# Kernel tuning notes

Measured on AMD Instinct MI355X. Metric: run time of the kernel, lower is better.

## Reference

```python
import jax, jax.numpy as jnp
import numpy as np

B, Tc, E, K, M, V = 8, 1024, 256, 8, 2048, 16
T1 = Tc * K          # penultimate layer length = 8192
TLAST = M * K        # last layer length = 16384


def setup_inputs() -> dict:
    key = jax.random.key(0)
    ks = jax.random.split(key, 12)
    x = jax.random.normal(ks[0], (B, Tc, E), jnp.float32)
    # penultimate values: exactly M 'mixed' tokens (value==2) per row, rest in {1,3}
    base = jnp.where(jnp.arange(T1) < M, 2, 1 + 2 * jax.random.randint(ks[1], (B, T1), 0, 2))
    perm = jnp.argsort(jax.random.uniform(ks[2], (B, T1)), axis=1)
    val1 = jnp.take_along_axis(base, perm, axis=1)
    vallast = 1 + 2 * jax.random.randint(ks[3], (B, TLAST), 0, 2)
    value = jnp.concatenate([val1, vallast], axis=1).astype(jnp.int64)
    depth = jnp.concatenate([jnp.full((B, T1), 5), jnp.full((B, TLAST), 6)], axis=1).astype(jnp.int64)
    pos = jax.random.randint(ks[4], (B, T1 + TLAST, 3), 0, 64).astype(jnp.int64)
    s = 0.02
    W1 = s * jax.random.normal(ks[5], (E, E, K), jnp.float32)  # ConvTranspose1d weight [in,out,k]
    b1 = s * jax.random.normal(ks[6], (E,), jnp.float32)
    W0 = s * jax.random.normal(ks[7], (E, E, K), jnp.float32)
    b0 = s * jax.random.normal(ks[8], (E,), jnp.float32)
    Wl = s * jax.random.normal(ks[9], (V + 1, E), jnp.float32)
    bl = s * jax.random.normal(ks[10], (V + 1,), jnp.float32)
    return {"x": x, "value": value, "depth": depth, "pos": pos, "num_mix": M,
            "W1": W1, "b1": b1, "W0": W0, "b0": b0, "Wl": Wl, "bl": bl}


def _deconv(x, W, b):
    # ConvTranspose1d with kernel=stride=K: each token expands to K tokens
    n, t, e = x.shape
    o = W.shape[1]
    y = jnp.einsum('nte,eoj->ntjo', x, W)  # [N,T,K,O]
    return y.reshape(n, t * W.shape[2], o) + b


def reference(x, value, depth, pos, num_mix, W1, b1, W0, b0, Wl, bl):
    n, tc, e = x.shape
    k = W1.shape[2]
    t1 = tc * k
    max_depth = jnp.max(depth)
    len_1 = jnp.sum(depth == max_depth - 1, axis=1)               # [N]
    tt = jnp.arange(t1)
    val_1 = jnp.where(tt[None, :] < len_1[:, None], value[:, :t1], 0)  # padded penultimate values
    mix_mask = val_1 == 2                                         # [N,T1]
    mix_1 = jnp.sum(mix_mask, axis=1)                             # [N]
    y_1 = _deconv(x, W1, b1)                                      # [N,T1,E]
    # stable pack: bring positions with value==2 to the front, keep order
    order = jnp.argsort(jnp.where(mix_mask, 0, 1), axis=1, stable=True)
    sel = order[:, :num_mix]                                      # [N,M]
    x_0 = jnp.take_along_axis(y_1, sel[:, :, None], axis=1)       # [N,M,E]
    valid = (jnp.arange(num_mix)[None, :] < mix_1[:, None]).astype(x_0.dtype)
    x_0 = x_0 * valid[:, :, None]                                 # zero-pad beyond per-row mix count
    y_0 = _deconv(x_0, W0, b0)                                    # [N,M*K,E]
    return y_0 @ Wl.T + bl                                        # [N,M*K,V+1]
```

## Files before the change

kernel.cpp:

```cpp
#include <hip/hip_runtime.h>

typedef __attribute__((ext_vector_type(8))) short bf16x8;
typedef __attribute__((ext_vector_type(4))) float f32x4;

#define BB 8
#define TC 1024
#define EE 256
#define KJ 8
#define MSEL 2048
#define V1 17
#define T1 8192
#define TTOT 24576
#define BI_TOT 16384
#define NCOLP 160
#define WSTRIDE 264

#define SCAL_OFF 0
#define GRP_OFF  1024
#define WFT_OFF  (GRP_OFF + 524288)
#define B2_OFF   (WFT_OFF + NCOLP*WSTRIDE*2)
#define BF0_OFF  (B2_OFF + 640)
#define WCT_OFF  (BF0_OFF + 128)

__device__ __forceinline__ unsigned short f2bf(float f) {
    union { float f; unsigned u; } x; x.f = f;
    unsigned r = x.u + 0x7fffu + ((x.u >> 16) & 1u);
    return (unsigned short)(r >> 16);
}
__device__ __forceinline__ float bf2f(unsigned short h) {
    union { unsigned u; float f; } x; x.u = ((unsigned)h) << 16;
    return x.f;
}

__global__ __launch_bounds__(256) void k_pre(const float* W0, const float* Wl, const int* depth,
                                             unsigned short* wfT, int* scal) {
    int bid = blockIdx.x, tid = threadIdx.x;
    __shared__ float w0s[EE * KJ];
    __shared__ float wls[V1 * 257];
    __shared__ int s_red[4];
    int em = bid;
    for (int idx = tid; idx < EE * KJ; idx += 256) w0s[idx] = W0[em * EE * KJ + idx];
    for (int idx = tid; idx < V1 * EE; idx += 256) {
        int v = idx >> 8, o = idx & 255;
        wls[v * 257 + o] = Wl[idx];
    }
    __syncthreads();
    if (tid < 136) {
        int j = tid / V1, v = tid - j * V1;
        float acc = 0.f;
        #pragma unroll 4
        for (int o = 0; o < EE; ++o) acc += w0s[o * KJ + j] * wls[v * 257 + o];
        wfT[(j * 20 + v) * WSTRIDE + em] = f2bf(acc);
    }
    if (bid < 8) {
        int b = bid;
        if (b == 0 && tid < 8) scal[33 + tid] = 0;
        const int4* dp = (const int4*)(depth + b * TTOT);
        int m = -2147483648;
        for (int i = tid; i < 6144; i += 256) {
            int4 d = dp[i];
            m = max(max(m, max(d.x, d.y)), max(d.z, d.w));
        }
        #pragma unroll
        for (int dd = 32; dd; dd >>= 1) m = max(m, __shfl_down(m, dd, 64));
        if ((tid & 63) == 0) s_red[tid >> 6] = m;
        __syncthreads();
        int bmax = max(max(s_red[0], s_red[1]), max(s_red[2], s_red[3]));
        if (tid == 0) scal[1 + b] = bmax;
        int c1 = 0, c2 = 0;
        for (int i = tid; i < 6144; i += 256) {
            int4 d = dp[i];
            c1 += (d.x == bmax) + (d.y == bmax) + (d.z == bmax) + (d.w == bmax);
            c2 += (d.x == bmax - 1) + (d.y == bmax - 1) + (d.z == bmax - 1) + (d.w == bmax - 1);
        }
        int cc = (c1 << 16) + c2;
        #pragma unroll
        for (int dd = 32; dd; dd >>= 1) cc += __shfl_down(cc, dd, 64);
        __syncthreads();
        if ((tid & 63) == 0) s_red[tid >> 6] = cc;
        __syncthreads();
        if (tid == 0) {
            int tot = s_red[0] + s_red[1] + s_red[2] + s_red[3];
            scal[9 + b] = tot >> 16;
            scal[17 + b] = tot & 0xffff;
        }
    }
}

__global__ __launch_bounds__(256) void k_mid(
        const int* value, const float* W1, const float* b1, const float* b0,
        const float* Wl, const float* bl,
        int* scal, int* groups, const unsigned short* wfT, float* bias2, float* bf0,
        unsigned short* wct) {
    int bid = blockIdx.x, tid = threadIdx.x;
    __shared__ __align__(16) unsigned short b1s[32 * WSTRIDE];
    __shared__ __align__(16) unsigned short af[NCOLP * WSTRIDE];
    __shared__ int s_wt[4], s_lcnt[8], s_lcnt2[8], s_lbase[8];
    if (bid < 64) {
        int g = bid >> 3;
        int e0 = (bid & 7) * 32;
        {
            int em_l = tid & 63;
            int eb = (tid >> 6) * 8;
            #pragma unroll
            for (int i = 0; i < 8; ++i) {
                int e = eb + i;
                #pragma unroll
                for (int c = 0; c < 4; ++c) {
                    int em = c * 64 + em_l;
                    b1s[e * WSTRIDE + em] = f2bf(W1[(e0 + e) * (EE * KJ) + em * KJ + g]);
                }
            }
        }
        for (int idx = tid; idx < 5120; idx += 256) {
            int row = idx >> 5, f = idx & 31;
            ((int4*)af)[row * 33 + f] = ((const int4*)wfT)[row * 33 + f];
        }
        __syncthreads();

        int w = tid >> 6, l = tid & 63;
        int ntile = w & 1, mhalf = w >> 1;
        int lr = l & 15, lq = l >> 4;
        f32x4 acc[5];
        #pragma unroll
        for (int t = 0; t < 5; ++t) acc[t] = (f32x4){0.f, 0.f, 0.f, 0.f};

        #pragma unroll
        for (int ch = 0; ch < 4; ++ch) {
            #pragma unroll
            for (int s = 0; s < 2; ++s) {
                bf16x8 bfr = *(const bf16x8*)&b1s[(ntile * 16 + lr) * WSTRIDE + ch * 64 + s * 32 + lq * 8];
                #pragma unroll
                for (int t = 0; t < 5; ++t) {
                    bf16x8 afr = *(const bf16x8*)&af[((mhalf * 5 + t) * 16 + lr) * WSTRIDE + ch * 64 + s * 32 + lq * 8];
                    acc[t] = __builtin_amdgcn_mfma_f32_16x16x32_bf16(afr, bfr, acc[t], 0, 0, 0);
                }
            }
        }
        #pragma unroll
        for (int t = 0; t < 5; ++t) {
            int m = (mhalf * 5 + t) * 16 + lq * 4;
            int n = e0 + ntile * 16 + lr;
            #pragma unroll
            for (int r = 0; r < 4; ++r)
                wct[(g * NCOLP + m + r) * WSTRIDE + n] = f2bf(acc[t][r]);
        }
        if (bid == 0) {
            for (int c = tid; c < NCOLP; c += 256) {
                int vv = c % 20;
                float s = 0.f;
                if (vv < V1) {
                    for (int e8 = 0; e8 < 32; ++e8) {
                        bf16x8 a8 = *(const bf16x8*)&af[c * WSTRIDE + e8 * 8];
                        #pragma unroll
                        for (int u = 0; u < 8; ++u)
                            s += b1[e8 * 8 + u] * bf2f((unsigned short)a8[u]);
                    }
                }
                bias2[c] = s;
            }
        } else if (bid == 1) {
            if (tid < V1) {
                float s = 0.f;
                #pragma unroll 4
                for (int e = 0; e < EE; ++e) s += b0[e] * Wl[tid * EE + e];
                bf0[tid] = s + bl[tid];
            }
        }
    } else {
        int b = bid - 64;
        int mb = scal[1 + b], cm = scal[9 + b], cm1 = scal[17 + b];
        int gmax = scal[1];
        #pragma unroll
        for (int q = 2; q <= 8; ++q) gmax = max(gmax, scal[q]);
        int len1 = (mb == gmax) ? cm1 : ((mb == gmax - 1) ? cm : 0);
        const int* vb = value + b * TTOT;
        int t0 = tid * 32;
        unsigned mask = 0;
        #pragma unroll
        for (int k = 0; k < 32; k += 4) {
            int4 v = *(const int4*)(vb + t0 + k);
            if (t0 + k + 0 < len1 && v.x == 2) mask |= 1u << (k + 0);
            if (t0 + k + 1 < len1 && v.y == 2) mask |= 1u << (k + 1);
            if (t0 + k + 2 < len1 && v.z == 2) mask |= 1u << (k + 2);
            if (t0 + k + 3 < len1 && v.w == 2) mask |= 1u << (k + 3);
        }
        int cnt = __popc(mask);
        int inc = cnt;
        #pragma unroll
        for (int d = 1; d < 64; d <<= 1) {
            int n = __shfl_up(inc, d, 64);
            if ((tid & 63) >= d) inc += n;
        }
        int lane = tid & 63, wid = tid >> 6;
        if (lane == 63) s_wt[wid] = inc;
        if (tid < 8) { s_lcnt[tid] = 0; s_lcnt2[tid] = 0; }
        __syncthreads();
        int woff = 0;
        for (int w = 0; w < wid; ++w) woff += s_wt[w];
        int off0 = woff + inc - cnt;
        int mix1 = s_wt[0] + s_wt[1] + s_wt[2] + s_wt[3];
        int mix1c = min(mix1, MSEL);
        {
            int off = off0;
            #pragma unroll
            for (int k = 0; k < 32; ++k) {
                if (mask & (1u << k)) {
                    if (off < MSEL) atomicAdd(&s_lcnt[(t0 + k) & 7], 1);
                    off++;
                }
            }
        }
        if (tid == 0 && mix1c < MSEL) atomicAdd(&s_lcnt[0], MSEL - mix1c);
        __syncthreads();
        if (tid < 8) s_lbase[tid] = atomicAdd(&scal[33 + tid], s_lcnt[tid]);
        __syncthreads();
        {
            int off = off0;
            #pragma unroll
            for (int k = 0; k < 32; ++k) {
                if (mask & (1u << k)) {
                    if (off < MSEL) {
                        int t = t0 + k;
                        int g = t & 7;
                        int ls = atomicAdd(&s_lcnt2[g], 1);
                        groups[g * BI_TOT + s_lbase[g] + ls] =
                            ((b * MSEL + off) << 11) | ((t >> 3) << 1) | 1;
                    }
                    off++;
                }
            }
        }
        for (int i = mix1c + tid; i < MSEL; i += 256) {
            int ls = atomicAdd(&s_lcnt2[0], 1);
            groups[s_lbase[0] + ls] = (b * MSEL + i) << 11;
        }
    }
}

__global__ __launch_bounds__(256) void k_main(const float* x, const unsigned short* wct,
        const int* scal, const int* groups, const float* bias2, const float* bf0, float* out) {
    int g = blockIdx.x >> 5;
    int slot = blockIdx.x & 31;
    int cntg = scal[33 + g];
    if (slot * 32 >= cntg) return;

    __shared__ __align__(16) unsigned short xs[32 * WSTRIDE];
    __shared__ __align__(16) unsigned short wts[NCOLP * WSTRIDE];
    __shared__ int xoffs[2][32], obase[2][32];
    __shared__ unsigned char vflag[2][32];
    int tid = threadIdx.x;
    const int4* wsrc = (const int4*)wct;

    if (tid < 32) {
        int nrows = min(32, cntg - slot * 32);
        int flag = 0, xo = 0, ob = 0;
        if (tid < nrows) {
            int pk = groups[g * BI_TOT + slot * 32 + tid];
            int tq = (pk >> 1) & 1023;
            int bi = pk >> 11;
            xo = ((bi >> 11) * TC + tq) * EE;
            ob = bi * 136;
            flag = 1 + (pk & 1);
        }
        xoffs[0][tid] = xo; obase[0][tid] = ob; vflag[0][tid] = (unsigned char)flag;
    }
    for (int idx = tid; idx < 5120; idx += 256) {
        int row = idx >> 5, f = idx & 31;
        ((int4*)wts)[row * 33 + f] = wsrc[(g * NCOLP + row) * 33 + f];
    }
    __syncthreads();

    int w = tid >> 6, l = tid & 63;
    int rw = w & 1, chalf = w >> 1;
    int lr = l & 15, lq = l >> 4;
    int row8 = tid >> 3, q8 = tid & 7;

    float4 xr[8];
    {
        const float* xp = x + xoffs[0][row8];
        #pragma unroll
        for (int i = 0; i < 8; ++i) xr[i] = *(const float4*)(xp + (q8 + 8 * i) * 4);
    }

    int pp = 0;
    for (int tile = slot; tile * 32 < cntg; tile += 32, pp ^= 1) {
        #pragma unroll
        for (int i = 0; i < 8; ++i) {
            ushort4 pk;
            pk.x = f2bf(xr[i].x); pk.y = f2bf(xr[i].y);
            pk.z = f2bf(xr[i].z); pk.w = f2bf(xr[i].w);
            *(ushort4*)&xs[row8 * WSTRIDE + (q8 + 8 * i) * 4] = pk;
        }
        int ntile = tile + 32;
        int more = (ntile * 32 < cntg);
        if (more && tid < 32) {
            int nrows = min(32, cntg - ntile * 32);
            int flag = 0, xo = 0, ob = 0;
            if (tid < nrows) {
                int pk = groups[g * BI_TOT + ntile * 32 + tid];
                int tq = (pk >> 1) & 1023;
                int bi = pk >> 11;
                xo = ((bi >> 11) * TC + tq) * EE;
                ob = bi * 136;
                flag = 1 + (pk & 1);
            }
            xoffs[pp ^ 1][tid] = xo; obase[pp ^ 1][tid] = ob; vflag[pp ^ 1][tid] = (unsigned char)flag;
        }
        __syncthreads();
        if (more) {
            const float* xp = x + xoffs[pp ^ 1][row8];
            #pragma unroll
            for (int i = 0; i < 8; ++i) xr[i] = *(const float4*)(xp + (q8 + 8 * i) * 4);
        }

        f32x4 acc[5];
        #pragma unroll
        for (int t = 0; t < 5; ++t) acc[t] = (f32x4){0.f, 0.f, 0.f, 0.f};
        #pragma unroll
        for (int ch = 0; ch < 4; ++ch) {
            #pragma unroll
            for (int s = 0; s < 2; ++s) {
                bf16x8 afr = *(const bf16x8*)&xs[(rw * 16 + lr) * WSTRIDE + ch * 64 + s * 32 + lq * 8];
                #pragma unroll
                for (int t = 0; t < 5; ++t) {
                    bf16x8 bfr = *(const bf16x8*)&wts[((chalf * 5 + t) * 16 + lr) * WSTRIDE + ch * 64 + s * 32 + lq * 8];
                    acc[t] = __builtin_amdgcn_mfma_f32_16x16x32_bf16(afr, bfr, acc[t], 0, 0, 0);
                }
            }
        }
        #pragma unroll
        for (int t = 0; t < 5; ++t) {
            int col = (chalf * 5 + t) * 16 + lr;
            int j = col / 20, v = col % 20;
            if (v < V1) {
                float bb = bias2[col] + bf0[v];
                float b0v = bf0[v];
                #pragma unroll
                for (int r = 0; r < 4; ++r) {
                    int row = rw * 16 + lq * 4 + r;
                    int fl = vflag[pp][row];
                    if (fl) out[obase[pp][row] + j * V1 + v] = (fl == 2) ? (acc[t][r] + bb) : b0v;
                }
            }
        }
        __syncthreads();
    }
}

extern "C" void kernel_launch(void* const* d_in, const int* in_sizes, int n_in,
                              void* d_out, int out_size, void* d_ws, size_t ws_size,
                              hipStream_t stream) {
    const float* x     = (const float*)d_in[0];
    const int*   value = (const int*)d_in[1];
    const int*   depth = (const int*)d_in[2];
    const float* W1    = (const float*)d_in[5];
    const float* b1    = (const float*)d_in[6];
    const float* W0    = (const float*)d_in[7];
    const float* b0    = (const float*)d_in[8];
    const float* Wl    = (const float*)d_in[9];
    const float* bl    = (const float*)d_in[10];
    float* out = (float*)d_out;
    char* ws = (char*)d_ws;

    int*            scal   = (int*)(ws + SCAL_OFF);
    int*            groups = (int*)(ws + GRP_OFF);
    unsigned short* wfT    = (unsigned short*)(ws + WFT_OFF);
    float*          bias2  = (float*)(ws + B2_OFF);
    float*          bf0    = (float*)(ws + BF0_OFF);
    unsigned short* wct    = (unsigned short*)(ws + WCT_OFF);

    k_pre <<<dim3(256), dim3(256), 0, stream>>>(W0, Wl, depth, wfT, scal);
    k_mid <<<dim3(72),  dim3(256), 0, stream>>>(value, W1, b1, b0, Wl, bl,
                                                scal, groups, wfT, bias2, bf0, wct);
    k_main<<<dim3(256), dim3(256), 0, stream>>>(x, wct, scal, groups, bias2, bf0, out);
}
```

Measured before the change: 131.8 us.

## Stream weight slices through small LDS buffer and quadruple k_main grid

k_main now launches 1024 blocks, 128 tiles per group, instead of 256. It no longer keeps the full 160x256 bf16 weight matrix resident in LDS. Instead it streams the weights in four 64-wide K chunks through a small LDS buffer, prefetching into registers and adding extra barriers. The smaller LDS footprint and larger grid are meant to raise occupancy and parallelism, at the cost of reloading weights for every tile, more synchronisation, and dropping the cross-tile x prefetch.

```diff
diff --git a/kernel.cpp b/kernel.cpp
--- a/kernel.cpp
+++ b/kernel.cpp
@@ -240,93 +240,79 @@
 
 __global__ __launch_bounds__(256) void k_main(const float* x, const unsigned short* wct,
         const int* scal, const int* groups, const float* bias2, const float* bf0, float* out) {
-    int g = blockIdx.x >> 5;
-    int slot = blockIdx.x & 31;
+    int g = blockIdx.x >> 7;
+    int tile0 = blockIdx.x & 127;
     int cntg = scal[33 + g];
-    if (slot * 32 >= cntg) return;
 
     __shared__ __align__(16) unsigned short xs[32 * WSTRIDE];
-    __shared__ __align__(16) unsigned short wts[NCOLP * WSTRIDE];
-    __shared__ int xoffs[2][32], obase[2][32];
-    __shared__ unsigned char vflag[2][32];
+    __shared__ __align__(16) unsigned short wts[NCOLP * 72];
+    __shared__ int obase[32];
+    __shared__ unsigned char vflag[32];
     int tid = threadIdx.x;
     const int4* wsrc = (const int4*)wct;
-
-    if (tid < 32) {
-        int nrows = min(32, cntg - slot * 32);
-        int flag = 0, xo = 0, ob = 0;
-        if (tid < nrows) {
-            int pk = groups[g * BI_TOT + slot * 32 + tid];
-            int tq = (pk >> 1) & 1023;
-            int bi = pk >> 11;
-            xo = ((bi >> 11) * TC + tq) * EE;
-            ob = bi * 136;
-            flag = 1 + (pk & 1);
-        }
-        xoffs[0][tid] = xo; obase[0][tid] = ob; vflag[0][tid] = (unsigned char)flag;
-    }
-    for (int idx = tid; idx < 5120; idx += 256) {
-        int row = idx >> 5, f = idx & 31;
-        ((int4*)wts)[row * 33 + f] = wsrc[(g * NCOLP + row) * 33 + f];
-    }
-    __syncthreads();
-
+    int row8 = tid >> 3, q8 = tid & 7;
     int w = tid >> 6, l = tid & 63;
     int rw = w & 1, chalf = w >> 1;
     int lr = l & 15, lq = l >> 4;
-    int row8 = tid >> 3, q8 = tid & 7;
-
-    float4 xr[8];
-    {
-        const float* xp = x + xoffs[0][row8];
-        #pragma unroll
-        for (int i = 0; i < 8; ++i) xr[i] = *(const float4*)(xp + (q8 + 8 * i) * 4);
-    }
-
-    int pp = 0;
-    for (int tile = slot; tile * 32 < cntg; tile += 32, pp ^= 1) {
+
+    for (int tile = tile0; tile * 32 < cntg; tile += 128) {
+        int nrows = min(32, cntg - tile * 32);
+        int4 wreg[5];
+        #pragma unroll
+        for (int q = 0; q < 5; ++q)
+            wreg[q] = wsrc[(g * NCOLP + row8 + q * 32) * 33 + q8];
+        int pk = (row8 < nrows) ? groups[g * BI_TOT + tile * 32 + row8] : 0;
+        int xo = ((pk >> 22) * TC + ((pk >> 1) & 1023)) * EE;
+        float4 xr[8];
+        #pragma unroll
+        for (int i = 0; i < 8; ++i) xr[i] = *(const float4*)(x + xo + (q8 + 8 * i) * 4);
+
+        __syncthreads();
+        if (tid < 32) {
+            int p2 = (tid < nrows) ? groups[g * BI_TOT + tile * 32 + tid] : 0;
+            obase[tid] = (p2 >> 11) * 136;
+            vflag[tid] = (tid < nrows) ? (unsigned char)(1 + (p2 & 1)) : (unsigned char)0;
+        }
         #pragma unroll
         for (int i = 0; i < 8; ++i) {
-            ushort4 pk;
-            pk.x = f2bf(xr[i].x); pk.y = f2bf(xr[i].y);
-            pk.z = f2bf(xr[i].z); pk.w = f2bf(xr[i].w);
-            *(ushort4*)&xs[row8 * WSTRIDE + (q8 + 8 * i) * 4] = pk;
-        }
-        int ntile = tile + 32;
-        int more = (ntile * 32 < cntg);
-        if (more && tid < 32) {
-            int nrows = min(32, cntg - ntile * 32);
-            int flag = 0, xo = 0, ob = 0;
-            if (tid < nrows) {
-                int pk = groups[g * BI_TOT + ntile * 32 + tid];
-                int tq = (pk >> 1) & 1023;
-                int bi = pk >> 11;
-                xo = ((bi >> 11) * TC + tq) * EE;
-                ob = bi * 136;
-                flag = 1 + (pk & 1);
-            }
-            xoffs[pp ^ 1][tid] = xo; obase[pp ^ 1][tid] = ob; vflag[pp ^ 1][tid] = (unsigned char)flag;
-        }
-        __syncthreads();
-        if (more) {
-            const float* xp = x + xoffs[pp ^ 1][row8];
-            #pragma unroll
-            for (int i = 0; i < 8; ++i) xr[i] = *(const float4*)(xp + (q8 + 8 * i) * 4);
-        }
+            ushort4 pkv;
+            pkv.x = f2bf(xr[i].x); pkv.y = f2bf(xr[i].y);
+            pkv.z = f2bf(xr[i].z); pkv.w = f2bf(xr[i].w);
+            *(ushort4*)&xs[row8 * WSTRIDE + (q8 + 8 * i) * 4] = pkv;
+        }
+        #pragma unroll
+        for (int q = 0; q < 5; ++q)
+            ((int4*)wts)[(row8 + q * 32) * 9 + q8] = wreg[q];
+        #pragma unroll
+        for (int q = 0; q < 5; ++q)
+            wreg[q] = wsrc[(g * NCOLP + row8 + q * 32) * 33 + 8 + q8];
+        __syncthreads();
 
         f32x4 acc[5];
         #pragma unroll
         for (int t = 0; t < 5; ++t) acc[t] = (f32x4){0.f, 0.f, 0.f, 0.f};
-        #pragma unroll
+
         for (int ch = 0; ch < 4; ++ch) {
             #pragma unroll
             for (int s = 0; s < 2; ++s) {
                 bf16x8 afr = *(const bf16x8*)&xs[(rw * 16 + lr) * WSTRIDE + ch * 64 + s * 32 + lq * 8];
                 #pragma unroll
                 for (int t = 0; t < 5; ++t) {
-                    bf16x8 bfr = *(const bf16x8*)&wts[((chalf * 5 + t) * 16 + lr) * WSTRIDE + ch * 64 + s * 32 + lq * 8];
+                    bf16x8 bfr = *(const bf16x8*)&wts[((chalf * 5 + t) * 16 + lr) * 72 + s * 32 + lq * 8];
                     acc[t] = __builtin_amdgcn_mfma_f32_16x16x32_bf16(afr, bfr, acc[t], 0, 0, 0);
                 }
+            }
+            if (ch < 3) {
+                __syncthreads();
+                #pragma unroll
+                for (int q = 0; q < 5; ++q)
+                    ((int4*)wts)[(row8 + q * 32) * 9 + q8] = wreg[q];
+                if (ch < 2) {
+                    #pragma unroll
+                    for (int q = 0; q < 5; ++q)
+                        wreg[q] = wsrc[(g * NCOLP + row8 + q * 32) * 33 + (ch + 2) * 8 + q8];
+                }
+                __syncthreads();
             }
         }
         #pragma unroll
@@ -339,12 +325,11 @@
                 #pragma unroll
                 for (int r = 0; r < 4; ++r) {
                     int row = rw * 16 + lq * 4 + r;
-                    int fl = vflag[pp][row];
-                    if (fl) out[obase[pp][row] + j * V1 + v] = (fl == 2) ? (acc[t][r] + bb) : b0v;
-                }
-            }
-        }
-        __syncthreads();
+                    int fl = vflag[row];
+                    if (fl) out[obase[row] + j * V1 + v] = (fl == 2) ? (acc[t][r] + bb) : b0v;
+                }
+            }
+        }
     }
 }
 
@@ -370,8 +355,8 @@
     float*          bf0    = (float*)(ws + BF0_OFF);
     unsigned short* wct    = (unsigned short*)(ws + WCT_OFF);
 
-    k_pre <<<dim3(256), dim3(256), 0, stream>>>(W0, Wl, depth, wfT, scal);
-    k_mid <<<dim3(72),  dim3(256), 0, stream>>>(value, W1, b1, b0, Wl, bl,
-                                                scal, groups, wfT, bias2, bf0, wct);
-    k_main<<<dim3(256), dim3(256), 0, stream>>>(x, wct, scal, groups, bias2, bf0, out);
-}
+    k_pre <<<dim3(256),  dim3(256), 0, stream>>>(W0, Wl, depth, wfT, scal);
+    k_mid <<<dim3(72),   dim3(256), 0, stream>>>(value, W1, b1, b0, Wl, bl,
+                                                 scal, groups, wfT, bias2, bf0, wct);
+    k_main<<<dim3(1024), dim3(256), 0, stream>>>(x, wct, scal, groups, bias2, bf0, out);
+}
```

Measured after the change: 137.5 us. 1.04x slower.
